# Performance work log

Hardware: AMD Instinct MI355X
Metric: run time of the kernel (lower is better)

The kernel has to match this reference:

```python
import jax, jax.numpy as jnp
import numpy as np

N, K, D = 131072, 1024, 256
COMMITMENT_COST = 0.25


def setup_inputs() -> dict:
    key = jax.random.key(0)
    k1, k2 = jax.random.split(key)
    z_e = jax.random.normal(k1, (N, D), dtype=jnp.float32)
    # matches nn.Embedding init: uniform(-1/K, 1/K)
    embedding = jax.random.uniform(k2, (K, D), dtype=jnp.float32,
                                   minval=-1.0 / K, maxval=1.0 / K)
    return {"z_e": z_e, "embedding": embedding}


def reference(z_e, embedding):
    # squared euclidean distances: [N, K]
    z_norm = jnp.sum(z_e * z_e, axis=1, keepdims=True)          # [N, 1]
    c_norm = jnp.sum(embedding * embedding, axis=1)             # [K]
    distances = z_norm + c_norm[None, :] - 2.0 * (z_e @ embedding.T)
    indices = jnp.argmin(distances, axis=1)                     # [N] int
    z_q = embedding[indices]                                    # gather [N, D]
    # commitment loss (the only loss the module returns)
    commitment_loss = COMMITMENT_COST * jnp.mean(
        (z_q - jax.lax.stop_gradient(z_e)) ** 2)
    # straight-through estimator
    z_q_st = z_e + jax.lax.stop_gradient(z_q - z_e)
    return z_q_st, indices, commitment_loss
```

## Files before the change

### kernel.cpp

```cpp
#include <hip/hip_runtime.h>

#define NROWS 131072
#define KCODES 1024
#define DDIM 256
#define BN 64
#define NBLK (NROWS / BN)
#define ZS 260
#define CTS 256
#define BKC 256
#define COMMIT 0.25

__device__ __forceinline__ float opaque(float x) {
    asm volatile("" : "+v"(x));
    return x;
}

__device__ __forceinline__ float elem4(const float4& v, int l) {
    switch (l) {
        case 0:  return v.x;
        case 1:  return v.y;
        case 2:  return v.z;
        default: return v.w;
    }
}

template <typename LD>
__device__ __forceinline__ float pairwise256_sq(LD ld) {
    float tt[2];
#pragma unroll
    for (int h = 0; h < 2; ++h) {
        float r[8];
#pragma unroll
        for (int j = 0; j < 8; ++j) {
            float e = ld(h * 128 + j);
            float p = e * e;
            p = opaque(p);
            r[j] = p;
        }
#pragma unroll
        for (int i = 1; i < 16; ++i) {
#pragma unroll
            for (int j = 0; j < 8; ++j) {
                float e = ld(h * 128 + i * 8 + j);
                float p = e * e;
                p = opaque(p);
                r[j] += p;
            }
        }
        tt[h] = ((r[0] + r[1]) + (r[2] + r[3])) + ((r[4] + r[5]) + (r[6] + r[7]));
    }
    return tt[0] + tt[1];
}

__global__ void cnorm_k(const float* __restrict__ emb, float* __restrict__ cn) {
    int code = blockIdx.x * blockDim.x + threadIdx.x;
    if (code >= KCODES) return;
    const float* x = emb + (size_t)code * DDIM;
    cn[code] = pairwise256_sq([&](int i) { return x[i]; });
}

__global__ __launch_bounds__(512, 2) void vq_main(
    const float* __restrict__ z_e, const float* __restrict__ emb,
    const float* __restrict__ cn_g, float* __restrict__ out_zq,
    float* __restrict__ out_idx, double* __restrict__ ws_part) {
    __shared__ float z_lds[BN * ZS];
    __shared__ float ct[64 * CTS];
    __shared__ float cn_l[KCODES];
    __shared__ float zn_l[BN];
    __shared__ int winner[BN];
    __shared__ double wsum[8];

    const int tid = threadIdx.x;
    const int bid = blockIdx.x;
    const size_t row0 = (size_t)bid * BN;

    {
        const float4* src = (const float4*)(z_e + row0 * DDIM);
#pragma unroll
        for (int q = 0; q < 8; ++q) {
            int g = q * 512 + tid;
            float4 v = src[g];
            int r = g >> 6, c4 = g & 63;
            *(float4*)&z_lds[r * ZS + c4 * 4] = v;
        }
        for (int i = tid; i < KCODES; i += 512) cn_l[i] = cn_g[i];
    }
    __syncthreads();

    if (tid < BN) {
        const float* x = &z_lds[tid * ZS];
        zn_l[tid] = pairwise256_sq([&](int i) { return x[i]; });
    }
    __syncthreads();

    const int ng = tid >> 5;
    const int tk = tid & 31;
    const int r0 = ng * 4;

    float mv[4];
    int mk[4];
#pragma unroll
    for (int i = 0; i < 4; ++i) {
        mv[i] = __builtin_inff();
        mk[i] = 0;
    }

    for (int k0 = 0; k0 < KCODES; k0 += BKC) {
        float acc[4][8];
#pragma unroll
        for (int i = 0; i < 4; ++i)
#pragma unroll
            for (int j = 0; j < 8; ++j) acc[i][j] = 0.0f;

        for (int dc = 0; dc < 4; ++dc) {
            __syncthreads();
            {
                int code = tid >> 1;
                int dh = (tid & 1) * 32;
                const float* sp = emb + (size_t)(k0 + code) * DDIM + dc * 64 + dh;
#pragma unroll
                for (int q = 0; q < 8; ++q) {
                    float4 v = *(const float4*)(sp + q * 4);
                    int d = dh + q * 4;
                    ct[(d + 0) * CTS + code] = v.x;
                    ct[(d + 1) * CTS + code] = v.y;
                    ct[(d + 2) * CTS + code] = v.z;
                    ct[(d + 3) * CTS + code] = v.w;
                }
            }
            __syncthreads();

            const float* zb0 = &z_lds[(r0 + 0) * ZS + dc * 64];
            const float* zb1 = &z_lds[(r0 + 1) * ZS + dc * 64];
            const float* zb2 = &z_lds[(r0 + 2) * ZS + dc * 64];
            const float* zb3 = &z_lds[(r0 + 3) * ZS + dc * 64];
            const float* cbA = &ct[tk * 4];
            const float* cbB = &ct[128 + tk * 4];

#pragma unroll
            for (int s = 0; s < 16; ++s) {
                float4 za0 = *(const float4*)(zb0 + s * 4);
                float4 za1 = *(const float4*)(zb1 + s * 4);
                float4 za2 = *(const float4*)(zb2 + s * 4);
                float4 za3 = *(const float4*)(zb3 + s * 4);
#pragma unroll
                for (int l = 0; l < 4; ++l) {
                    float4 cA = *(const float4*)(cbA + (s * 4 + l) * CTS);
                    float4 cB = *(const float4*)(cbB + (s * 4 + l) * CTS);
                    float zl[4] = {elem4(za0, l), elem4(za1, l), elem4(za2, l), elem4(za3, l)};
#pragma unroll
                    for (int i = 0; i < 4; ++i) {
#pragma unroll
                        for (int j = 0; j < 4; ++j) {
                            acc[i][j] = __builtin_fmaf(zl[i], elem4(cA, j), acc[i][j]);
                            acc[i][4 + j] = __builtin_fmaf(zl[i], elem4(cB, j), acc[i][4 + j]);
                        }
                    }
                }
            }
        }

        float zn[4];
#pragma unroll
        for (int i = 0; i < 4; ++i) zn[i] = zn_l[r0 + i];
#pragma unroll
        for (int j = 0; j < 8; ++j) {
            int kk = k0 + ((j < 4) ? (tk * 4 + j) : (128 + tk * 4 + (j - 4)));
            float c = cn_l[kk];
#pragma unroll
            for (int i = 0; i < 4; ++i) {
                float t1 = zn[i] + c;
                float dv = t1 - 2.0f * acc[i][j];
                if (dv < mv[i] || (dv == mv[i] && kk < mk[i])) {
                    mv[i] = dv;
                    mk[i] = kk;
                }
            }
        }
    }

    __syncthreads();
    float* red_v = ct;
    int* red_k = (int*)(ct + 64 * 33);
#pragma unroll
    for (int i = 0; i < 4; ++i) {
        red_v[(r0 + i) * 33 + tk] = mv[i];
        red_k[(r0 + i) * 33 + tk] = mk[i];
    }
    __syncthreads();
    if (tid < BN) {
        float bv = red_v[tid * 33];
        int bk = red_k[tid * 33];
        for (int t = 1; t < 32; ++t) {
            float v = red_v[tid * 33 + t];
            int k = red_k[tid * 33 + t];
            if (v < bv || (v == bv && k < bk)) {
                bv = v;
                bk = k;
            }
        }
        winner[tid] = bk;
        out_idx[row0 + tid] = (float)bk;
    }
    __syncthreads();

    double lsum = 0.0;
    {
        int row = tid >> 3;
        int seg = (tid & 7) * 32;
        int kk = winner[row];
        const float* zq = emb + (size_t)kk * DDIM + seg;
        const float* zz = &z_lds[row * ZS + seg];
        float4* dst = (float4*)(out_zq + (row0 + row) * DDIM + seg);
#pragma unroll
        for (int q = 0; q < 8; ++q) {
            float4 a = *(const float4*)(zq + q * 4);
            float4 b = *(const float4*)(zz + q * 4);
            float s0 = a.x - b.x, s1 = a.y - b.y, s2 = a.z - b.z, s3 = a.w - b.w;
            float4 o;
            o.x = b.x + s0;
            o.y = b.y + s1;
            o.z = b.z + s2;
            o.w = b.w + s3;
            dst[q] = o;
            float q0 = s0 * s0, q1 = s1 * s1, q2 = s2 * s2, q3 = s3 * s3;
            lsum += (double)q0 + (double)q1 + (double)q2 + (double)q3;
        }
    }
#pragma unroll
    for (int off = 32; off > 0; off >>= 1) lsum += __shfl_down(lsum, off);
    if ((tid & 63) == 0) wsum[tid >> 6] = lsum;
    __syncthreads();
    if (tid == 0) {
        double t = 0.0;
#pragma unroll
        for (int w = 0; w < 8; ++w) t += wsum[w];
        ws_part[bid] = t;
    }
}

__global__ void loss_k(const double* __restrict__ part, float* __restrict__ out_loss) {
    __shared__ double wsum[8];
    int tid = threadIdx.x;
    double s = 0.0;
    for (int i = tid; i < NBLK; i += 512) s += part[i];
#pragma unroll
    for (int off = 32; off > 0; off >>= 1) s += __shfl_down(s, off);
    if ((tid & 63) == 0) wsum[tid >> 6] = s;
    __syncthreads();
    if (tid == 0) {
        double t = 0.0;
#pragma unroll
        for (int w = 0; w < 8; ++w) t += wsum[w];
        out_loss[0] = (float)(COMMIT * (t / ((double)NROWS * (double)DDIM)));
    }
}

extern "C" void kernel_launch(void* const* d_in, const int* in_sizes, int n_in,
                              void* d_out, int out_size, void* d_ws, size_t ws_size,
                              hipStream_t stream) {
    const float* z_e = (const float*)d_in[0];
    const float* emb = (const float*)d_in[1];
    float* out = (float*)d_out;
    float* out_zq = out;
    float* out_idx = out + (size_t)NROWS * DDIM;
    float* out_loss = out_idx + NROWS;

    double* part = (double*)d_ws;
    float* cn_g = (float*)((char*)d_ws + NBLK * sizeof(double));

    cnorm_k<<<4, 256, 0, stream>>>(emb, cn_g);
    vq_main<<<NBLK, 512, 0, stream>>>(z_e, emb, cn_g, out_zq, out_idx, part);
    loss_k<<<1, 512, 0, stream>>>(part, out_loss);
}
```

Before: 1.394 ms.

## Restructure VQ distance kernel: per-wave rows, double-buffered codebook tiles, shuffle argmin

Each wave now owns 8 rows and reads z directly from global memory (wave-uniform broadcast loads) instead of staging the whole z block in LDS. The codebook is streamed in 16-dim slices into a double-buffered, padded LDS tile so only one barrier is needed per slice. Argmin is reduced with wave shuffles rather than through LDS. The smaller LDS footprint allows 4 blocks per SM. The cost is many more barriers and per-slice global loads of z, and each thread's register tile changes to 8 rows x 4 codes.

Result: slower. 2.795 ms (+100.5%).

```diff
diff --git a/kernel.cpp b/kernel.cpp
--- a/kernel.cpp
+++ b/kernel.cpp
@@ -5,23 +5,15 @@
 #define DDIM 256
 #define BN 64
 #define NBLK (NROWS / BN)
-#define ZS 260
-#define CTS 256
-#define BKC 256
+#define RW 8
+#define SC 256
+#define NCH (KCODES / SC)
+#define STR 20
 #define COMMIT 0.25
 
-__device__ __forceinline__ float opaque(float x) {
+__device__ __forceinline__ float opq(float x) {
     asm volatile("" : "+v"(x));
     return x;
-}
-
-__device__ __forceinline__ float elem4(const float4& v, int l) {
-    switch (l) {
-        case 0:  return v.x;
-        case 1:  return v.y;
-        case 2:  return v.z;
-        default: return v.w;
-    }
 }
 
 template <typename LD>
@@ -34,7 +26,7 @@
         for (int j = 0; j < 8; ++j) {
             float e = ld(h * 128 + j);
             float p = e * e;
-            p = opaque(p);
+            p = opq(p);
             r[j] = p;
         }
 #pragma unroll
@@ -43,7 +35,7 @@
             for (int j = 0; j < 8; ++j) {
                 float e = ld(h * 128 + i * 8 + j);
                 float p = e * e;
-                p = opaque(p);
+                p = opq(p);
                 r[j] += p;
             }
         }
@@ -59,177 +51,165 @@
     cn[code] = pairwise256_sq([&](int i) { return x[i]; });
 }
 
-__global__ __launch_bounds__(512, 2) void vq_main(
+__global__ __launch_bounds__(512, 4) void vq_main(
     const float* __restrict__ z_e, const float* __restrict__ emb,
     const float* __restrict__ cn_g, float* __restrict__ out_zq,
     float* __restrict__ out_idx, double* __restrict__ ws_part) {
-    __shared__ float z_lds[BN * ZS];
-    __shared__ float ct[64 * CTS];
-    __shared__ float cn_l[KCODES];
-    __shared__ float zn_l[BN];
-    __shared__ int winner[BN];
+    __shared__ float ctb[2][SC * STR];
     __shared__ double wsum[8];
 
     const int tid = threadIdx.x;
+    const int lane = tid & 63;
+    const int wid = __builtin_amdgcn_readfirstlane(tid >> 6);
     const int bid = blockIdx.x;
-    const size_t row0 = (size_t)bid * BN;
-
-    {
-        const float4* src = (const float4*)(z_e + row0 * DDIM);
-#pragma unroll
-        for (int q = 0; q < 8; ++q) {
-            int g = q * 512 + tid;
-            float4 v = src[g];
-            int r = g >> 6, c4 = g & 63;
-            *(float4*)&z_lds[r * ZS + c4 * 4] = v;
-        }
-        for (int i = tid; i < KCODES; i += 512) cn_l[i] = cn_g[i];
-    }
-    __syncthreads();
-
-    if (tid < BN) {
-        const float* x = &z_lds[tid * ZS];
-        zn_l[tid] = pairwise256_sq([&](int i) { return x[i]; });
-    }
-    __syncthreads();
-
-    const int ng = tid >> 5;
-    const int tk = tid & 31;
-    const int r0 = ng * 4;
-
-    float mv[4];
-    int mk[4];
-#pragma unroll
-    for (int i = 0; i < 4; ++i) {
-        mv[i] = __builtin_inff();
-        mk[i] = 0;
-    }
-
-    for (int k0 = 0; k0 < KCODES; k0 += BKC) {
-        float acc[4][8];
-#pragma unroll
-        for (int i = 0; i < 4; ++i)
-#pragma unroll
-            for (int j = 0; j < 8; ++j) acc[i][j] = 0.0f;
-
-        for (int dc = 0; dc < 4; ++dc) {
+    const size_t row0 = (size_t)bid * BN + (size_t)wid * RW;
+
+    float zn = 0.0f;
+    if (lane < 8) {
+        const float* x = z_e + (row0 + lane) * DDIM;
+        float tt[2];
+#pragma unroll
+        for (int h = 0; h < 2; ++h) {
+            float r8[8];
+            {
+                float4 a = *(const float4*)(x + h * 128);
+                float4 b = *(const float4*)(x + h * 128 + 4);
+                r8[0] = opq(a.x * a.x); r8[1] = opq(a.y * a.y);
+                r8[2] = opq(a.z * a.z); r8[3] = opq(a.w * a.w);
+                r8[4] = opq(b.x * b.x); r8[5] = opq(b.y * b.y);
+                r8[6] = opq(b.z * b.z); r8[7] = opq(b.w * b.w);
+            }
+#pragma unroll
+            for (int i = 1; i < 16; ++i) {
+                float4 a = *(const float4*)(x + h * 128 + i * 8);
+                float4 b = *(const float4*)(x + h * 128 + i * 8 + 4);
+                r8[0] += opq(a.x * a.x); r8[1] += opq(a.y * a.y);
+                r8[2] += opq(a.z * a.z); r8[3] += opq(a.w * a.w);
+                r8[4] += opq(b.x * b.x); r8[5] += opq(b.y * b.y);
+                r8[6] += opq(b.z * b.z); r8[7] += opq(b.w * b.w);
+            }
+            tt[h] = ((r8[0] + r8[1]) + (r8[2] + r8[3])) + ((r8[4] + r8[5]) + (r8[6] + r8[7]));
+        }
+        zn = tt[0] + tt[1];
+    }
+    float znb[8];
+#pragma unroll
+    for (int r = 0; r < 8; ++r) znb[r] = __shfl(zn, r);
+
+    float mv[8];
+    int mk[8];
+#pragma unroll
+    for (int r = 0; r < 8; ++r) {
+        mv[r] = __builtin_inff();
+        mk[r] = 0;
+    }
+
+    const int cc = tid >> 1;
+    const int hh = tid & 1;
+
+    for (int ch = 0; ch < NCH; ++ch) {
+        const int code0 = ch * SC;
+        float acc[8][4];
+#pragma unroll
+        for (int r = 0; r < 8; ++r)
+#pragma unroll
+            for (int m = 0; m < 4; ++m) acc[r][m] = 0.0f;
+
+        {
+            const float* sp = emb + (size_t)(code0 + cc) * DDIM + hh * 8;
+            float4 a = *(const float4*)sp;
+            float4 b = *(const float4*)(sp + 4);
+            float* dp = &ctb[0][cc * STR + hh * 8];
+            *(float4*)dp = a;
+            *(float4*)(dp + 4) = b;
+        }
+
+        for (int db = 0; db < 16; ++db) {
             __syncthreads();
-            {
-                int code = tid >> 1;
-                int dh = (tid & 1) * 32;
-                const float* sp = emb + (size_t)(k0 + code) * DDIM + dc * 64 + dh;
-#pragma unroll
-                for (int q = 0; q < 8; ++q) {
-                    float4 v = *(const float4*)(sp + q * 4);
-                    int d = dh + q * 4;
-                    ct[(d + 0) * CTS + code] = v.x;
-                    ct[(d + 1) * CTS + code] = v.y;
-                    ct[(d + 2) * CTS + code] = v.z;
-                    ct[(d + 3) * CTS + code] = v.w;
-                }
-            }
-            __syncthreads();
-
-            const float* zb0 = &z_lds[(r0 + 0) * ZS + dc * 64];
-            const float* zb1 = &z_lds[(r0 + 1) * ZS + dc * 64];
-            const float* zb2 = &z_lds[(r0 + 2) * ZS + dc * 64];
-            const float* zb3 = &z_lds[(r0 + 3) * ZS + dc * 64];
-            const float* cbA = &ct[tk * 4];
-            const float* cbB = &ct[128 + tk * 4];
-
-#pragma unroll
-            for (int s = 0; s < 16; ++s) {
-                float4 za0 = *(const float4*)(zb0 + s * 4);
-                float4 za1 = *(const float4*)(zb1 + s * 4);
-                float4 za2 = *(const float4*)(zb2 + s * 4);
-                float4 za3 = *(const float4*)(zb3 + s * 4);
-#pragma unroll
-                for (int l = 0; l < 4; ++l) {
-                    float4 cA = *(const float4*)(cbA + (s * 4 + l) * CTS);
-                    float4 cB = *(const float4*)(cbB + (s * 4 + l) * CTS);
-                    float zl[4] = {elem4(za0, l), elem4(za1, l), elem4(za2, l), elem4(za3, l)};
-#pragma unroll
-                    for (int i = 0; i < 4; ++i) {
-#pragma unroll
-                        for (int j = 0; j < 4; ++j) {
-                            acc[i][j] = __builtin_fmaf(zl[i], elem4(cA, j), acc[i][j]);
-                            acc[i][4 + j] = __builtin_fmaf(zl[i], elem4(cB, j), acc[i][4 + j]);
-                        }
+            if (db + 1 < 16) {
+                const float* sp = emb + (size_t)(code0 + cc) * DDIM + (db + 1) * 16 + hh * 8;
+                float4 a = *(const float4*)sp;
+                float4 b = *(const float4*)(sp + 4);
+                float* dp = &ctb[(db + 1) & 1][cc * STR + hh * 8];
+                *(float4*)dp = a;
+                *(float4*)(dp + 4) = b;
+            }
+            const float* cb = &ctb[db & 1][lane * STR];
+            const float* zb = z_e + row0 * DDIM + db * 16;
+#pragma unroll
+            for (int j4 = 0; j4 < 4; ++j4) {
+                float4 zv[8];
+#pragma unroll
+                for (int r = 0; r < 8; ++r)
+                    zv[r] = *(const float4*)(zb + r * DDIM + j4 * 4);
+#pragma unroll
+                for (int m = 0; m < 4; ++m) {
+                    float4 cv = *(const float4*)(cb + m * 64 * STR + j4 * 4);
+#pragma unroll
+                    for (int r = 0; r < 8; ++r) {
+                        acc[r][m] = __builtin_fmaf(zv[r].x, cv.x, acc[r][m]);
+                        acc[r][m] = __builtin_fmaf(zv[r].y, cv.y, acc[r][m]);
+                        acc[r][m] = __builtin_fmaf(zv[r].z, cv.z, acc[r][m]);
+                        acc[r][m] = __builtin_fmaf(zv[r].w, cv.w, acc[r][m]);
                     }
                 }
             }
         }
 
-        float zn[4];
-#pragma unroll
-        for (int i = 0; i < 4; ++i) zn[i] = zn_l[r0 + i];
-#pragma unroll
-        for (int j = 0; j < 8; ++j) {
-            int kk = k0 + ((j < 4) ? (tk * 4 + j) : (128 + tk * 4 + (j - 4)));
-            float c = cn_l[kk];
-#pragma unroll
-            for (int i = 0; i < 4; ++i) {
-                float t1 = zn[i] + c;
-                float dv = t1 - 2.0f * acc[i][j];
-                if (dv < mv[i] || (dv == mv[i] && kk < mk[i])) {
-                    mv[i] = dv;
-                    mk[i] = kk;
+#pragma unroll
+        for (int m = 0; m < 4; ++m) {
+            const int kk = code0 + m * 64 + lane;
+            const float cno = cn_g[kk];
+#pragma unroll
+            for (int r = 0; r < 8; ++r) {
+                float t1 = znb[r] + cno;
+                float dv = t1 - 2.0f * acc[r][m];
+                if (dv < mv[r] || (dv == mv[r] && kk < mk[r])) {
+                    mv[r] = dv;
+                    mk[r] = kk;
                 }
             }
         }
     }
 
-    __syncthreads();
-    float* red_v = ct;
-    int* red_k = (int*)(ct + 64 * 33);
-#pragma unroll
-    for (int i = 0; i < 4; ++i) {
-        red_v[(r0 + i) * 33 + tk] = mv[i];
-        red_k[(r0 + i) * 33 + tk] = mk[i];
-    }
-    __syncthreads();
-    if (tid < BN) {
-        float bv = red_v[tid * 33];
-        int bk = red_k[tid * 33];
-        for (int t = 1; t < 32; ++t) {
-            float v = red_v[tid * 33 + t];
-            int k = red_k[tid * 33 + t];
-            if (v < bv || (v == bv && k < bk)) {
-                bv = v;
-                bk = k;
-            }
-        }
-        winner[tid] = bk;
-        out_idx[row0 + tid] = (float)bk;
-    }
-    __syncthreads();
+#pragma unroll
+    for (int r = 0; r < 8; ++r) {
+        float bv = mv[r];
+        int bk = mk[r];
+#pragma unroll
+        for (int off = 1; off < 64; off <<= 1) {
+            float ov = __shfl_xor(bv, off);
+            int ok = __shfl_xor(bk, off);
+            if (ov < bv || (ov == bv && ok < bk)) {
+                bv = ov;
+                bk = ok;
+            }
+        }
+        mv[r] = bv;
+        mk[r] = bk;
+    }
+    if (lane == 0) {
+#pragma unroll
+        for (int r = 0; r < 8; ++r) out_idx[row0 + r] = (float)mk[r];
+    }
 
     double lsum = 0.0;
-    {
-        int row = tid >> 3;
-        int seg = (tid & 7) * 32;
-        int kk = winner[row];
-        const float* zq = emb + (size_t)kk * DDIM + seg;
-        const float* zz = &z_lds[row * ZS + seg];
-        float4* dst = (float4*)(out_zq + (row0 + row) * DDIM + seg);
-#pragma unroll
-        for (int q = 0; q < 8; ++q) {
-            float4 a = *(const float4*)(zq + q * 4);
-            float4 b = *(const float4*)(zz + q * 4);
-            float s0 = a.x - b.x, s1 = a.y - b.y, s2 = a.z - b.z, s3 = a.w - b.w;
-            float4 o;
-            o.x = b.x + s0;
-            o.y = b.y + s1;
-            o.z = b.z + s2;
-            o.w = b.w + s3;
-            dst[q] = o;
-            float q0 = s0 * s0, q1 = s1 * s1, q2 = s2 * s2, q3 = s3 * s3;
-            lsum += (double)q0 + (double)q1 + (double)q2 + (double)q3;
-        }
+#pragma unroll
+    for (int r = 0; r < 8; ++r) {
+        const float4 a = *(const float4*)(emb + (size_t)mk[r] * DDIM + lane * 4);
+        const float4 b = *(const float4*)(z_e + (row0 + r) * DDIM + lane * 4);
+        float s0 = a.x - b.x, s1 = a.y - b.y, s2 = a.z - b.z, s3 = a.w - b.w;
+        float4 o;
+        o.x = b.x + s0;
+        o.y = b.y + s1;
+        o.z = b.z + s2;
+        o.w = b.w + s3;
+        *(float4*)(out_zq + (row0 + r) * DDIM + lane * 4) = o;
+        lsum += (double)(s0 * s0) + (double)(s1 * s1) + (double)(s2 * s2) + (double)(s3 * s3);
     }
 #pragma unroll
     for (int off = 32; off > 0; off >>= 1) lsum += __shfl_down(lsum, off);
-    if ((tid & 63) == 0) wsum[tid >> 6] = lsum;
+    if (lane == 0) wsum[wid] = lsum;
     __syncthreads();
     if (tid == 0) {
         double t = 0.0;
```

## Retile distance GEMM to 8x8 register blocks with double-buffered D-slices

Applied to the files above, without the earlier changes.

Restructures the main distance computation. Each thread now holds an 8x8 register tile of rows by codes, and work is split into two 512-code chunks. The D dimension is streamed in 16-wide slices through double-buffered padded shared memory, so the global load of the next slice overlaps compute on the current one and the transposing scatter store goes away. The argmin reduction now uses wavefront xor-shuffles followed by a small cross-wave pass, and z is re-read from global memory for the output stage instead of being kept whole in shared memory. The costs are higher register pressure from 64 accumulators and two z tiles being reloaded, once per code chunk.

Measured after the change: 1.359 ms. 2.5% less time.

```diff
diff --git a/kernel.cpp b/kernel.cpp
--- a/kernel.cpp
+++ b/kernel.cpp
@@ -5,171 +5,156 @@
 #define DDIM 256
 #define BN 64
 #define NBLK (NROWS / BN)
-#define ZS 260
-#define CTS 256
-#define BKC 256
+#define CHUNK 512
+#define STR 20
 #define COMMIT 0.25
 
-__device__ __forceinline__ float opaque(float x) {
+__device__ __forceinline__ float opq(float x) {
     asm volatile("" : "+v"(x));
     return x;
 }
 
-__device__ __forceinline__ float elem4(const float4& v, int l) {
-    switch (l) {
-        case 0:  return v.x;
-        case 1:  return v.y;
-        case 2:  return v.z;
-        default: return v.w;
-    }
-}
-
-template <typename LD>
-__device__ __forceinline__ float pairwise256_sq(LD ld) {
-    float tt[2];
-#pragma unroll
-    for (int h = 0; h < 2; ++h) {
-        float r[8];
+__device__ __forceinline__ float half128_sq(const float* __restrict__ x) {
+    float r[8];
+#pragma unroll
+    for (int j = 0; j < 8; ++j) {
+        float e = x[j];
+        float p = e * e;
+        p = opq(p);
+        r[j] = p;
+    }
+#pragma unroll
+    for (int i = 1; i < 16; ++i) {
 #pragma unroll
         for (int j = 0; j < 8; ++j) {
-            float e = ld(h * 128 + j);
+            float e = x[i * 8 + j];
             float p = e * e;
-            p = opaque(p);
-            r[j] = p;
-        }
-#pragma unroll
-        for (int i = 1; i < 16; ++i) {
-#pragma unroll
-            for (int j = 0; j < 8; ++j) {
-                float e = ld(h * 128 + i * 8 + j);
-                float p = e * e;
-                p = opaque(p);
-                r[j] += p;
-            }
-        }
-        tt[h] = ((r[0] + r[1]) + (r[2] + r[3])) + ((r[4] + r[5]) + (r[6] + r[7]));
-    }
-    return tt[0] + tt[1];
+            p = opq(p);
+            r[j] += p;
+        }
+    }
+    return ((r[0] + r[1]) + (r[2] + r[3])) + ((r[4] + r[5]) + (r[6] + r[7]));
 }
 
 __global__ void cnorm_k(const float* __restrict__ emb, float* __restrict__ cn) {
     int code = blockIdx.x * blockDim.x + threadIdx.x;
     if (code >= KCODES) return;
     const float* x = emb + (size_t)code * DDIM;
-    cn[code] = pairwise256_sq([&](int i) { return x[i]; });
+    cn[code] = half128_sq(x) + half128_sq(x + 128);
 }
 
 __global__ __launch_bounds__(512, 2) void vq_main(
     const float* __restrict__ z_e, const float* __restrict__ emb,
     const float* __restrict__ cn_g, float* __restrict__ out_zq,
     float* __restrict__ out_idx, double* __restrict__ ws_part) {
-    __shared__ float z_lds[BN * ZS];
-    __shared__ float ct[64 * CTS];
+    __shared__ float c_s[2][CHUNK * STR];
+    __shared__ float z_s[2][BN * STR];
     __shared__ float cn_l[KCODES];
+    __shared__ float znh[BN][2];
     __shared__ float zn_l[BN];
+    __shared__ float red_v[8][BN];
+    __shared__ int red_k[8][BN];
     __shared__ int winner[BN];
     __shared__ double wsum[8];
 
     const int tid = threadIdx.x;
+    const int lane = tid & 63;
+    const int wv = __builtin_amdgcn_readfirstlane(tid >> 6);
+    const int r8 = lane >> 3;
+    const int c8 = lane & 7;
     const int bid = blockIdx.x;
     const size_t row0 = (size_t)bid * BN;
 
-    {
-        const float4* src = (const float4*)(z_e + row0 * DDIM);
-#pragma unroll
-        for (int q = 0; q < 8; ++q) {
-            int g = q * 512 + tid;
-            float4 v = src[g];
-            int r = g >> 6, c4 = g & 63;
-            *(float4*)&z_lds[r * ZS + c4 * 4] = v;
-        }
-        for (int i = tid; i < KCODES; i += 512) cn_l[i] = cn_g[i];
-    }
-    __syncthreads();
-
-    if (tid < BN) {
-        const float* x = &z_lds[tid * ZS];
-        zn_l[tid] = pairwise256_sq([&](int i) { return x[i]; });
-    }
-    __syncthreads();
-
-    const int ng = tid >> 5;
-    const int tk = tid & 31;
-    const int r0 = ng * 4;
-
-    float mv[4];
-    int mk[4];
-#pragma unroll
-    for (int i = 0; i < 4; ++i) {
+    for (int i = tid; i < KCODES; i += 512) cn_l[i] = cn_g[i];
+    if (tid < 128) {
+        int row = tid >> 1, h = tid & 1;
+        znh[row][h] = half128_sq(z_e + (row0 + row) * DDIM + h * 128);
+    }
+    __syncthreads();
+    if (tid < BN) zn_l[tid] = znh[tid][0] + znh[tid][1];
+
+    float mv[8];
+    int mk[8];
+#pragma unroll
+    for (int i = 0; i < 8; ++i) {
         mv[i] = __builtin_inff();
         mk[i] = 0;
     }
 
-    for (int k0 = 0; k0 < KCODES; k0 += BKC) {
-        float acc[4][8];
-#pragma unroll
-        for (int i = 0; i < 4; ++i)
+    for (int ch = 0; ch < 2; ++ch) {
+        const int code0 = ch * CHUNK;
+        float acc[8][8];
+#pragma unroll
+        for (int i = 0; i < 8; ++i)
 #pragma unroll
             for (int j = 0; j < 8; ++j) acc[i][j] = 0.0f;
 
-        for (int dc = 0; dc < 4; ++dc) {
+        {
+#pragma unroll
+            for (int q = 0; q < 4; ++q) {
+                int g = q * 512 + tid;
+                int code = g >> 2, off = (g & 3) * 4;
+                float4 v = *(const float4*)(emb + (size_t)(code0 + code) * DDIM + off);
+                *(float4*)&c_s[0][code * STR + off] = v;
+            }
+            if (tid < 256) {
+                int row = tid >> 2, off = (tid & 3) * 4;
+                float4 v = *(const float4*)(z_e + (row0 + row) * DDIM + off);
+                *(float4*)&z_s[0][row * STR + off] = v;
+            }
+        }
+
+        for (int st = 0; st < 16; ++st) {
             __syncthreads();
-            {
-                int code = tid >> 1;
-                int dh = (tid & 1) * 32;
-                const float* sp = emb + (size_t)(k0 + code) * DDIM + dc * 64 + dh;
-#pragma unroll
-                for (int q = 0; q < 8; ++q) {
-                    float4 v = *(const float4*)(sp + q * 4);
-                    int d = dh + q * 4;
-                    ct[(d + 0) * CTS + code] = v.x;
-                    ct[(d + 1) * CTS + code] = v.y;
-                    ct[(d + 2) * CTS + code] = v.z;
-                    ct[(d + 3) * CTS + code] = v.w;
+            if (st + 1 < 16) {
+                const int nb = (st + 1) & 1, d0 = (st + 1) * 16;
+#pragma unroll
+                for (int q = 0; q < 4; ++q) {
+                    int g = q * 512 + tid;
+                    int code = g >> 2, off = (g & 3) * 4;
+                    float4 v = *(const float4*)(emb + (size_t)(code0 + code) * DDIM + d0 + off);
+                    *(float4*)&c_s[nb][code * STR + off] = v;
                 }
-            }
-            __syncthreads();
-
-            const float* zb0 = &z_lds[(r0 + 0) * ZS + dc * 64];
-            const float* zb1 = &z_lds[(r0 + 1) * ZS + dc * 64];
-            const float* zb2 = &z_lds[(r0 + 2) * ZS + dc * 64];
-            const float* zb3 = &z_lds[(r0 + 3) * ZS + dc * 64];
-            const float* cbA = &ct[tk * 4];
-            const float* cbB = &ct[128 + tk * 4];
-
-#pragma unroll
-            for (int s = 0; s < 16; ++s) {
-                float4 za0 = *(const float4*)(zb0 + s * 4);
-                float4 za1 = *(const float4*)(zb1 + s * 4);
-                float4 za2 = *(const float4*)(zb2 + s * 4);
-                float4 za3 = *(const float4*)(zb3 + s * 4);
-#pragma unroll
-                for (int l = 0; l < 4; ++l) {
-                    float4 cA = *(const float4*)(cbA + (s * 4 + l) * CTS);
-                    float4 cB = *(const float4*)(cbB + (s * 4 + l) * CTS);
-                    float zl[4] = {elem4(za0, l), elem4(za1, l), elem4(za2, l), elem4(za3, l)};
-#pragma unroll
-                    for (int i = 0; i < 4; ++i) {
-#pragma unroll
-                        for (int j = 0; j < 4; ++j) {
-                            acc[i][j] = __builtin_fmaf(zl[i], elem4(cA, j), acc[i][j]);
-                            acc[i][4 + j] = __builtin_fmaf(zl[i], elem4(cB, j), acc[i][4 + j]);
-                        }
+                if (tid < 256) {
+                    int row = tid >> 2, off = (tid & 3) * 4;
+                    float4 v = *(const float4*)(z_e + (row0 + row) * DDIM + d0 + off);
+                    *(float4*)&z_s[nb][row * STR + off] = v;
+                }
+            }
+            const int cb = st & 1;
+            const float* cbase = &c_s[cb][(wv * 64 + c8) * STR];
+            const float* zbase = &z_s[cb][r8 * STR];
+#pragma unroll
+            for (int l4 = 0; l4 < 4; ++l4) {
+                float4 zv[8], cv[8];
+#pragma unroll
+                for (int i = 0; i < 8; ++i)
+                    zv[i] = *(const float4*)(zbase + i * 8 * STR + l4 * 4);
+#pragma unroll
+                for (int j = 0; j < 8; ++j)
+                    cv[j] = *(const float4*)(cbase + j * 8 * STR + l4 * 4);
+#pragma unroll
+                for (int i = 0; i < 8; ++i)
+#pragma unroll
+                    for (int j = 0; j < 8; ++j) {
+                        acc[i][j] = __builtin_fmaf(zv[i].x, cv[j].x, acc[i][j]);
+                        acc[i][j] = __builtin_fmaf(zv[i].y, cv[j].y, acc[i][j]);
+                        acc[i][j] = __builtin_fmaf(zv[i].z, cv[j].z, acc[i][j]);
+                        acc[i][j] = __builtin_fmaf(zv[i].w, cv[j].w, acc[i][j]);
                     }
-                }
-            }
-        }
-
-        float zn[4];
-#pragma unroll
-        for (int i = 0; i < 4; ++i) zn[i] = zn_l[r0 + i];
+            }
+        }
+
+        float znr[8];
+#pragma unroll
+        for (int i = 0; i < 8; ++i) znr[i] = zn_l[r8 + i * 8];
 #pragma unroll
         for (int j = 0; j < 8; ++j) {
-            int kk = k0 + ((j < 4) ? (tk * 4 + j) : (128 + tk * 4 + (j - 4)));
-            float c = cn_l[kk];
-#pragma unroll
-            for (int i = 0; i < 4; ++i) {
-                float t1 = zn[i] + c;
+            const int kk = code0 + wv * 64 + j * 8 + c8;
+            const float cno = cn_l[kk];
+#pragma unroll
+            for (int i = 0; i < 8; ++i) {
+                float t1 = znr[i] + cno;
                 float dv = t1 - 2.0f * acc[i][j];
                 if (dv < mv[i] || (dv == mv[i] && kk < mk[i])) {
                     mv[i] = dv;
@@ -179,21 +164,32 @@
         }
     }
 
-    __syncthreads();
-    float* red_v = ct;
-    int* red_k = (int*)(ct + 64 * 33);
-#pragma unroll
-    for (int i = 0; i < 4; ++i) {
-        red_v[(r0 + i) * 33 + tk] = mv[i];
-        red_k[(r0 + i) * 33 + tk] = mk[i];
+#pragma unroll
+    for (int i = 0; i < 8; ++i) {
+        float bv = mv[i];
+        int bk = mk[i];
+#pragma unroll
+        for (int off = 1; off < 8; off <<= 1) {
+            float ov = __shfl_xor(bv, off);
+            int ok = __shfl_xor(bk, off);
+            if (ov < bv || (ov == bv && ok < bk)) {
+                bv = ov;
+                bk = ok;
+            }
+        }
+        if (c8 == 0) {
+            red_v[wv][r8 + i * 8] = bv;
+            red_k[wv][r8 + i * 8] = bk;
+        }
     }
     __syncthreads();
     if (tid < BN) {
-        float bv = red_v[tid * 33];
-        int bk = red_k[tid * 33];
-        for (int t = 1; t < 32; ++t) {
-            float v = red_v[tid * 33 + t];
-            int k = red_k[tid * 33 + t];
+        float bv = red_v[0][tid];
+        int bk = red_k[0][tid];
+#pragma unroll
+        for (int w = 1; w < 8; ++w) {
+            float v = red_v[w][tid];
+            int k = red_k[w][tid];
             if (v < bv || (v == bv && k < bk)) {
                 bv = v;
                 bk = k;
@@ -210,7 +206,7 @@
         int seg = (tid & 7) * 32;
         int kk = winner[row];
         const float* zq = emb + (size_t)kk * DDIM + seg;
-        const float* zz = &z_lds[row * ZS + seg];
+        const float* zz = z_e + (row0 + row) * DDIM + seg;
         float4* dst = (float4*)(out_zq + (row0 + row) * DDIM + seg);
 #pragma unroll
         for (int q = 0; q < 8; ++q) {
@@ -223,13 +219,12 @@
             o.z = b.z + s2;
             o.w = b.w + s3;
             dst[q] = o;
-            float q0 = s0 * s0, q1 = s1 * s1, q2 = s2 * s2, q3 = s3 * s3;
-            lsum += (double)q0 + (double)q1 + (double)q2 + (double)q3;
+            lsum += (double)(s0 * s0) + (double)(s1 * s1) + (double)(s2 * s2) + (double)(s3 * s3);
         }
     }
 #pragma unroll
     for (int off = 32; off > 0; off >>= 1) lsum += __shfl_down(lsum, off);
-    if ((tid & 63) == 0) wsum[tid >> 6] = lsum;
+    if (lane == 0) wsum[wv] = lsum;
     __syncthreads();
     if (tid == 0) {
         double t = 0.0;
```
